# Optimization experiments

Hardware: AMD Instinct MI355X
Metric: run time of the kernel (lower is better)

Reference implementation:

```python
import jax, jax.numpy as jnp
import numpy as np
import math

B, N, D_IN, D_V, H, D_FF = 8, 2048, 256, 256, 8, 512
HD = D_V // H  # head dim = 32
EPS = 1e-5


def layernorm(x, g, b):
    mu = jnp.mean(x, axis=-1, keepdims=True)
    var = jnp.mean(jnp.square(x - mu), axis=-1, keepdims=True)
    return (x - mu) * jax.lax.rsqrt(var + EPS) * g + b


def setup_inputs() -> dict:
    key = jax.random.key(0)
    ks = jax.random.split(key, 12)
    s = 1.0 / math.sqrt(D_IN)
    return {
        "x": jax.random.normal(ks[0], (B, N, D_IN), jnp.float32),
        "y": jax.random.normal(ks[1], (B, N, D_IN), jnp.float32),
        "Wq": jax.random.normal(ks[2], (D_IN, D_V), jnp.float32) * s,
        "bq": jnp.zeros((D_V,), jnp.float32),
        "Wk": jax.random.normal(ks[3], (D_IN, D_V), jnp.float32) * s,
        "bk": jnp.zeros((D_V,), jnp.float32),
        "Wv": jax.random.normal(ks[4], (D_IN, D_V), jnp.float32) * s,
        "bv": jnp.zeros((D_V,), jnp.float32),
        "W1": jax.random.normal(ks[5], (D_V, D_FF), jnp.float32) * s,
        "b1": jnp.zeros((D_FF,), jnp.float32),
        "W2": jax.random.normal(ks[6], (D_FF, D_V), jnp.float32) * (1.0 / math.sqrt(D_FF)),
        "b2": jnp.zeros((D_V,), jnp.float32),
        "ln0_g": jnp.ones((D_IN,), jnp.float32),
        "ln0_b": jnp.zeros((D_IN,), jnp.float32),
        "ln1_g": jnp.ones((D_V,), jnp.float32),
        "ln1_b": jnp.zeros((D_V,), jnp.float32),
    }


def reference(x, y, Wq, bq, Wk, bk, Wv, bv, W1, b1, W2, b2, ln0_g, ln0_b, ln1_g, ln1_b):
    xn = layernorm(x, ln0_g, ln0_b)                      # ln0 on queries
    Q = (xn @ Wq + bq).reshape(B, N, H, HD)              # [B,Nq,H,hd]
    K = (y @ Wk + bk).reshape(B, N, H, HD)
    V = (y @ Wv + bv).reshape(B, N, H, HD)
    # NOTE: faithful scale = 1/sqrt(dim_V) (full model dim), not head dim
    S = jnp.einsum("bqhd,bkhd->bhqk", Q, K) / math.sqrt(D_V)
    A = jax.nn.softmax(S, axis=-1)
    O = Q + jnp.einsum("bhqk,bkhd->bqhd", A, V)          # per-head residual Q_ + A
    O = O.reshape(B, N, D_V)
    On = layernorm(O, ln1_g, ln1_b)
    ff = jax.nn.gelu(On @ W1 + b1, approximate=False) @ W2 + b2
    return O + ff
```

## Files before the change

kernel.cpp:

```cpp
#include <hip/hip_runtime.h>
#include <math.h>

#define RTOT 16384
#define NSEQ 2048
#define NHEAD 8
#define HDIM 32
#define QSCALE 0.09017132252479462f
#define QINV (1.0f / QSCALE)

typedef __attribute__((ext_vector_type(8))) short short8;
typedef __attribute__((ext_vector_type(4))) float f32x4;

#define GLOBAL_AS(p) ((__attribute__((address_space(1))) void*)(p))
#define LDS_AS(p) ((__attribute__((address_space(3))) void*)(p))

__device__ __forceinline__ unsigned pack_bf16(float a, float b) {
  unsigned ua = __float_as_uint(a) + 0x8000u;
  unsigned ub = __float_as_uint(b) + 0x8000u;
  return (ua >> 16) | (ub & 0xffff0000u);
}
__device__ __forceinline__ unsigned pack_bf16_perm(float a, float b) {
  return __builtin_amdgcn_perm(__float_as_uint(b), __float_as_uint(a),
                               0x07060302u);
}
__device__ __forceinline__ ushort bf16_1(float a) {
  return (ushort)((__float_as_uint(a) + 0x8000u) >> 16);
}
__device__ __forceinline__ float bf16_to_f(ushort u) {
  return __uint_as_float(((unsigned)u) << 16);
}

__global__ __launch_bounds__(256) void stage0_kernel(
    const float* __restrict__ x, const float* __restrict__ y,
    const float* __restrict__ Wq, const float* __restrict__ Wk,
    const float* __restrict__ Wv, const float* __restrict__ W1,
    const float* __restrict__ W2, const float* __restrict__ ln0g,
    const float* __restrict__ ln0b, ushort* __restrict__ Wqt,
    ushort* __restrict__ Wkt, ushort* __restrict__ Wvt,
    ushort* __restrict__ W1t, ushort* __restrict__ W2t,
    ushort* __restrict__ yh, ushort* __restrict__ xh) {
  const int bid = blockIdx.x;
  const int t = threadIdx.x;
  if (bid < 112) {
    const float* W;
    ushort* Wt;
    int K, N, tile;
    if (bid < 16) { W = Wq; Wt = Wqt; K = 256; N = 256; tile = bid; }
    else if (bid < 32) { W = Wk; Wt = Wkt; K = 256; N = 256; tile = bid - 16; }
    else if (bid < 48) { W = Wv; Wt = Wvt; K = 256; N = 256; tile = bid - 32; }
    else if (bid < 80) { W = W1; Wt = W1t; K = 256; N = 512; tile = bid - 48; }
    else { W = W2; Wt = W2t; K = 512; N = 256; tile = bid - 80; }
    const int tn = N >> 6;
    const int k0 = (tile / tn) << 6, n0 = (tile % tn) << 6;
    __shared__ float T[64][65];
#pragma unroll
    for (int i = 0; i < 16; ++i) {
      const int idx = t + i * 256;
      const int r = idx >> 6, c = idx & 63;
      T[r][c] = W[(size_t)(k0 + r) * N + n0 + c];
    }
    __syncthreads();
#pragma unroll
    for (int i = 0; i < 16; ++i) {
      const int idx = t + i * 256;
      const int r = idx >> 6, c = idx & 63;
      Wt[(size_t)(n0 + r) * K + k0 + c] = bf16_1(T[c][r]);
    }
  } else if (bid < 4208) {
    const size_t i = ((size_t)(bid - 112) * 256 + t) * 4;
    const float4 v = *(const float4*)&y[i];
    uint2 pk;
    pk.x = pack_bf16(v.x, v.y);
    pk.y = pack_bf16(v.z, v.w);
    *(uint2*)&yh[i] = pk;
  } else {
    const int lane = t & 63, wave = t >> 6;
    const size_t row = (size_t)(bid - 4208) * 4 + wave;
    const float* xr = x + row * 256;
    float4 v = *(const float4*)&xr[lane * 4];
    float s = v.x + v.y + v.z + v.w;
#pragma unroll
    for (int m = 1; m < 64; m <<= 1) s += __shfl_xor(s, m, 64);
    const float mu = s * (1.0f / 256.0f);
    const float dx = v.x - mu, dy = v.y - mu, dz = v.z - mu, dw = v.w - mu;
    float ss = dx * dx + dy * dy + dz * dz + dw * dw;
#pragma unroll
    for (int m = 1; m < 64; m <<= 1) ss += __shfl_xor(ss, m, 64);
    const float rstd = rsqrtf(ss * (1.0f / 256.0f) + 1e-5f);
    const float4 gv = *(const float4*)&ln0g[lane * 4];
    const float4 bv = *(const float4*)&ln0b[lane * 4];
    uint2 pk;
    pk.x = pack_bf16(dx * rstd * gv.x + bv.x, dy * rstd * gv.y + bv.y);
    pk.y = pack_bf16(dz * rstd * gv.z + bv.z, dw * rstd * gv.w + bv.w);
    *(uint2*)&xh[row * 256 + lane * 4] = pk;
  }
}

__global__ __launch_bounds__(256) void ln_kernel(
    const float* __restrict__ X, const float* __restrict__ g,
    const float* __restrict__ bt, ushort* __restrict__ Yh) {
  const int lane = threadIdx.x & 63;
  const int wave = threadIdx.x >> 6;
  const size_t row = (size_t)blockIdx.x * 4 + wave;
  const float* xr = X + row * 256;
  float4 v = *(const float4*)&xr[lane * 4];
  float s = v.x + v.y + v.z + v.w;
#pragma unroll
  for (int m = 1; m < 64; m <<= 1) s += __shfl_xor(s, m, 64);
  const float mu = s * (1.0f / 256.0f);
  const float dx = v.x - mu, dy = v.y - mu, dz = v.z - mu, dw = v.w - mu;
  float ss = dx * dx + dy * dy + dz * dz + dw * dw;
#pragma unroll
  for (int m = 1; m < 64; m <<= 1) ss += __shfl_xor(ss, m, 64);
  const float rstd = rsqrtf(ss * (1.0f / 256.0f) + 1e-5f);
  const float4 gv = *(const float4*)&g[lane * 4];
  const float4 bv = *(const float4*)&bt[lane * 4];
  uint2 pk;
  pk.x = pack_bf16(dx * rstd * gv.x + bv.x, dy * rstd * gv.y + bv.y);
  pk.y = pack_bf16(dz * rstd * gv.z + bv.z, dw * rstd * gv.w + bv.w);
  *(uint2*)&Yh[row * 256 + lane * 4] = pk;
}

__global__ __launch_bounds__(256) void qkv_kernel(
    const ushort* __restrict__ xh, const ushort* __restrict__ yh,
    const ushort* __restrict__ Wqt, const ushort* __restrict__ Wkt,
    const ushort* __restrict__ Wvt, const float* __restrict__ bq,
    const float* __restrict__ bk, const float* __restrict__ bv,
    ushort* __restrict__ Qh, ushort* __restrict__ Kh,
    ushort* __restrict__ VhT) {
  __shared__ union UU {
    struct { ushort As[128 * 32]; ushort Bs[64 * 32]; } s;
    ushort Ct[64 * 136];
  } u;
  const int t = threadIdx.x;
  const int lane = t & 63, wave = t >> 6;
  const int l16 = lane & 15, quad = lane >> 4;
  const int row0 = blockIdx.x * 128;
  const int ny = blockIdx.y;
  const int which = ny >> 2;
  const int n0 = (ny & 3) << 6;
  const ushort* A = (which == 2) ? xh : yh;
  const ushort* W = (which == 0) ? Wkt : (which == 1) ? Wvt : Wqt;
  const float* bs = (which == 0) ? bk : (which == 1) ? bv : bq;
  const int mrow = (wave & 1) * 64, ncol = (wave >> 1) * 32;

  const ushort* gA0 = A + (size_t)(row0 + (t >> 2)) * 256 + ((t & 3) << 3);
  const ushort* gA1 = gA0 + (size_t)64 * 256;
  const ushort* gB = W + (size_t)(n0 + (t >> 2)) * 256 + ((t & 3) << 3);
  ushort* lA0 = u.s.As + 8 * t;
  ushort* lA1 = u.s.As + 2048 + 8 * t;
  ushort* lB = u.s.Bs + 8 * t;

  f32x4 acc[4][2] = {};
  for (int kc = 0; kc < 256; kc += 32) {
    __builtin_amdgcn_global_load_lds(GLOBAL_AS(gA0 + kc), LDS_AS(lA0), 16, 0, 0);
    __builtin_amdgcn_global_load_lds(GLOBAL_AS(gA1 + kc), LDS_AS(lA1), 16, 0, 0);
    __builtin_amdgcn_global_load_lds(GLOBAL_AS(gB + kc), LDS_AS(lB), 16, 0, 0);
    __syncthreads();
    short8 af[4], bfr[2];
#pragma unroll
    for (int mi = 0; mi < 4; ++mi)
      af[mi] = *(const short8*)&u.s.As[(mrow + mi * 16 + l16) * 32 + quad * 8];
#pragma unroll
    for (int nj = 0; nj < 2; ++nj)
      bfr[nj] = *(const short8*)&u.s.Bs[(ncol + nj * 16 + l16) * 32 + quad * 8];
#pragma unroll
    for (int mi = 0; mi < 4; ++mi)
#pragma unroll
      for (int nj = 0; nj < 2; ++nj)
        acc[mi][nj] = __builtin_amdgcn_mfma_f32_16x16x32_bf16(
            af[mi], bfr[nj], acc[mi][nj], 0, 0, 0);
    __syncthreads();
  }

  if (which == 1) {
#pragma unroll
    for (int nj = 0; nj < 2; ++nj) {
      const int nloc = ncol + nj * 16 + l16;
      const float bvv = bs[n0 + nloc];
#pragma unroll
      for (int mi = 0; mi < 4; ++mi)
#pragma unroll
        for (int r = 0; r < 4; ++r)
          u.Ct[nloc * 136 + mrow + mi * 16 + quad * 4 + r] =
              bf16_1(acc[mi][nj][r] + bvv);
    }
    __syncthreads();
    const int bb = row0 >> 11, ns0 = row0 & 2047;
#pragma unroll
    for (int i = 0; i < 4; ++i) {
      const int c = t + i * 256;
      const int rr = c >> 4, c8 = (c & 15) << 3;
      *(float4*)&VhT[(size_t)(bb * 256 + n0 + rr) * 2048 + ns0 + c8] =
          *(const float4*)&u.Ct[rr * 136 + c8];
    }
  } else {
#pragma unroll
    for (int nj = 0; nj < 2; ++nj) {
      const int n = n0 + ncol + nj * 16 + l16;
      const float bvv = bs[n];
#pragma unroll
      for (int mi = 0; mi < 4; ++mi) {
#pragma unroll
        for (int r = 0; r < 4; ++r) {
          const size_t m = (size_t)row0 + mrow + mi * 16 + quad * 4 + r;
          const float v = acc[mi][nj][r] + bvv;
          if (which == 2) Qh[m * 256 + n] = bf16_1(v * QSCALE);
          else Kh[m * 256 + n] = bf16_1(v);
        }
      }
    }
  }
}

template <int MODE>
__global__ __launch_bounds__(256) void mgemm_kernel(
    const ushort* __restrict__ A, const ushort* __restrict__ Wt,
    const float* __restrict__ bias, const float* __restrict__ res,
    float* __restrict__ Cf, ushort* __restrict__ Ch, int K, int N) {
  __shared__ ushort As[128 * 32];
  __shared__ ushort Bs[64 * 32];
  const int t = threadIdx.x;
  const int lane = t & 63, wave = t >> 6;
  const int l16 = lane & 15, quad = lane >> 4;
  const int row0 = blockIdx.x * 128;
  const int n0 = blockIdx.y << 6;
  const int mrow = (wave & 1) * 64, ncol = (wave >> 1) * 32;

  const ushort* gA0 = A + (size_t)(row0 + (t >> 2)) * K + ((t & 3) << 3);
  const ushort* gA1 = gA0 + (size_t)64 * K;
  const ushort* gB = Wt + (size_t)(n0 + (t >> 2)) * K + ((t & 3) << 3);
  ushort* lA0 = As + 8 * t;
  ushort* lA1 = As + 2048 + 8 * t;
  ushort* lB = Bs + 8 * t;

  f32x4 acc[4][2] = {};
  for (int kc = 0; kc < K; kc += 32) {
    __builtin_amdgcn_global_load_lds(GLOBAL_AS(gA0 + kc), LDS_AS(lA0), 16, 0, 0);
    __builtin_amdgcn_global_load_lds(GLOBAL_AS(gA1 + kc), LDS_AS(lA1), 16, 0, 0);
    __builtin_amdgcn_global_load_lds(GLOBAL_AS(gB + kc), LDS_AS(lB), 16, 0, 0);
    __syncthreads();
    short8 af[4], bfr[2];
#pragma unroll
    for (int mi = 0; mi < 4; ++mi)
      af[mi] = *(const short8*)&As[(mrow + mi * 16 + l16) * 32 + quad * 8];
#pragma unroll
    for (int nj = 0; nj < 2; ++nj)
      bfr[nj] = *(const short8*)&Bs[(ncol + nj * 16 + l16) * 32 + quad * 8];
#pragma unroll
    for (int mi = 0; mi < 4; ++mi)
#pragma unroll
      for (int nj = 0; nj < 2; ++nj)
        acc[mi][nj] = __builtin_amdgcn_mfma_f32_16x16x32_bf16(
            af[mi], bfr[nj], acc[mi][nj], 0, 0, 0);
    __syncthreads();
  }
#pragma unroll
  for (int nj = 0; nj < 2; ++nj) {
    const int n = n0 + ncol + nj * 16 + l16;
    const float bvv = bias[n];
#pragma unroll
    for (int mi = 0; mi < 4; ++mi) {
#pragma unroll
      for (int r = 0; r < 4; ++r) {
        const size_t m = (size_t)row0 + mrow + mi * 16 + quad * 4 + r;
        float v = acc[mi][nj][r] + bvv;
        if (MODE == 2) {
          v = 0.5f * v * (1.0f + erff(v * 0.70710678118654752f));
          Ch[m * N + n] = bf16_1(v);
        }
        if (MODE == 3) Cf[m * N + n] = v + res[m * N + n];
      }
    }
  }
}

__global__ __launch_bounds__(256) void attn_kernel(
    const ushort* __restrict__ Qh, const ushort* __restrict__ Kh,
    const ushort* __restrict__ VhT, float* __restrict__ O) {
  __shared__ ushort Ks[2][64][40];
  __shared__ ushort Vt[2][32][72];
  __shared__ ushort Pl[4][2][16][72];

  const int t = threadIdx.x;
  const int lane = t & 63, wave = t >> 6;
  const int l16 = lane & 15, quad = lane >> 4;
  const int bh = blockIdx.x & 63;
  const int qt = blockIdx.x >> 6;
  const int b = bh >> 3, h = bh & 7;

  const size_t rowQ0 = (size_t)(b * NSEQ + qt * 128 + wave * 32 + l16);
  const short8 qfrag0 = *(const short8*)&Qh[rowQ0 * 256 + h * HDIM + quad * 8];
  const short8 qfrag1 =
      *(const short8*)&Qh[(rowQ0 + 16) * 256 + h * HDIM + quad * 8];
  const short8 ones = {16256, 16256, 16256, 16256,
                       16256, 16256, 16256, 16256};
  const f32x4 zf = {0.f, 0.f, 0.f, 0.f};

  f32x4 o00 = zf, o01 = zf, o10 = zf, o11 = zf;
  f32x4 s0 = zf, s1 = zf;

  const int kr = t >> 2, kc8 = (t & 3) << 3;
  const int vd = t >> 3, vc8 = (t & 7) << 3;
  const ushort* gK = Kh + ((size_t)(b * NSEQ + kr)) * 256 + h * HDIM + kc8;
  const ushort* gV = VhT + ((size_t)(bh * 32 + vd)) * 2048 + vc8;

  float4 kreg = *(const float4*)gK;
  float4 vreg = *(const float4*)gV;

  for (int kt = 0; kt < 32; ++kt) {
    const int bf = kt & 1;
    *(float4*)&Ks[bf][kr][kc8] = kreg;
    *(float4*)&Vt[bf][vd][vc8] = vreg;
    __syncthreads();
    if (kt < 31) {
      kreg = *(const float4*)(gK + (size_t)(kt + 1) * 64 * 256);
      vreg = *(const float4*)(gV + (kt + 1) * 64);
    }

    short8 kf[4];
#pragma unroll
    for (int sub = 0; sub < 4; ++sub)
      kf[sub] = *(const short8*)&Ks[bf][sub * 16 + l16][quad * 8];
    const short8 vf00 = *(const short8*)&Vt[bf][l16][quad * 8];
    const short8 vf01 = *(const short8*)&Vt[bf][l16][32 + quad * 8];
    const short8 vf10 = *(const short8*)&Vt[bf][16 + l16][quad * 8];
    const short8 vf11 = *(const short8*)&Vt[bf][16 + l16][32 + quad * 8];

    f32x4 sa0[4], sa1[4];
#pragma unroll
    for (int sub = 0; sub < 4; ++sub)
      sa0[sub] =
          __builtin_amdgcn_mfma_f32_16x16x32_bf16(kf[sub], qfrag0, zf, 0, 0, 0);
#pragma unroll
    for (int sub = 0; sub < 4; ++sub)
      sa1[sub] =
          __builtin_amdgcn_mfma_f32_16x16x32_bf16(kf[sub], qfrag1, zf, 0, 0, 0);

#pragma unroll
    for (int sub = 0; sub < 4; ++sub) {
      uint2 pk;
      pk.x = pack_bf16_perm(__builtin_amdgcn_exp2f(sa0[sub][0]),
                            __builtin_amdgcn_exp2f(sa0[sub][1]));
      pk.y = pack_bf16_perm(__builtin_amdgcn_exp2f(sa0[sub][2]),
                            __builtin_amdgcn_exp2f(sa0[sub][3]));
      *(uint2*)&Pl[wave][0][l16][sub * 16 + quad * 4] = pk;
    }
#pragma unroll
    for (int sub = 0; sub < 4; ++sub) {
      uint2 pk;
      pk.x = pack_bf16_perm(__builtin_amdgcn_exp2f(sa1[sub][0]),
                            __builtin_amdgcn_exp2f(sa1[sub][1]));
      pk.y = pack_bf16_perm(__builtin_amdgcn_exp2f(sa1[sub][2]),
                            __builtin_amdgcn_exp2f(sa1[sub][3]));
      *(uint2*)&Pl[wave][1][l16][sub * 16 + quad * 4] = pk;
    }
    __threadfence_block();

    const short8 pf00 = *(const short8*)&Pl[wave][0][l16][quad * 8];
    const short8 pf01 = *(const short8*)&Pl[wave][0][l16][32 + quad * 8];
    const short8 pf10 = *(const short8*)&Pl[wave][1][l16][quad * 8];
    const short8 pf11 = *(const short8*)&Pl[wave][1][l16][32 + quad * 8];
    o00 = __builtin_amdgcn_mfma_f32_16x16x32_bf16(pf00, vf00, o00, 0, 0, 0);
    o00 = __builtin_amdgcn_mfma_f32_16x16x32_bf16(pf01, vf01, o00, 0, 0, 0);
    o01 = __builtin_amdgcn_mfma_f32_16x16x32_bf16(pf00, vf10, o01, 0, 0, 0);
    o01 = __builtin_amdgcn_mfma_f32_16x16x32_bf16(pf01, vf11, o01, 0, 0, 0);
    o10 = __builtin_amdgcn_mfma_f32_16x16x32_bf16(pf10, vf00, o10, 0, 0, 0);
    o10 = __builtin_amdgcn_mfma_f32_16x16x32_bf16(pf11, vf01, o10, 0, 0, 0);
    o11 = __builtin_amdgcn_mfma_f32_16x16x32_bf16(pf10, vf10, o11, 0, 0, 0);
    o11 = __builtin_amdgcn_mfma_f32_16x16x32_bf16(pf11, vf11, o11, 0, 0, 0);
    s0 = __builtin_amdgcn_mfma_f32_16x16x32_bf16(pf00, ones, s0, 0, 0, 0);
    s0 = __builtin_amdgcn_mfma_f32_16x16x32_bf16(pf01, ones, s0, 0, 0, 0);
    s1 = __builtin_amdgcn_mfma_f32_16x16x32_bf16(pf10, ones, s1, 0, 0, 0);
    s1 = __builtin_amdgcn_mfma_f32_16x16x32_bf16(pf11, ones, s1, 0, 0, 0);
  }

  __threadfence_block();
  *(short8*)&Pl[wave][0][l16][quad * 8] = qfrag0;
  *(short8*)&Pl[wave][1][l16][quad * 8] = qfrag1;
  __threadfence_block();
#pragma unroll
  for (int g = 0; g < 2; ++g) {
    const f32x4 oS = g ? s1 : s0;
    const f32x4 oa = g ? o10 : o00;
    const f32x4 ob = g ? o11 : o01;
    const size_t row0 =
        (size_t)(b * NSEQ + qt * 128 + wave * 32 + g * 16 + quad * 4);
#pragma unroll
    for (int r = 0; r < 4; ++r) {
      const float q0 = bf16_to_f(Pl[wave][g][quad * 4 + r][l16]) * QINV;
      const float q1 = bf16_to_f(Pl[wave][g][quad * 4 + r][16 + l16]) * QINV;
      const float il = 1.0f / oS[r];
      const size_t ro = (row0 + r) * 256 + h * HDIM + l16;
      O[ro] = q0 + oa[r] * il;
      O[ro + 16] = q1 + ob[r] * il;
    }
  }
}

extern "C" void kernel_launch(void* const* d_in, const int* in_sizes, int n_in,
                              void* d_out, int out_size, void* d_ws, size_t ws_size,
                              hipStream_t stream) {
  const float* x = (const float*)d_in[0];
  const float* y = (const float*)d_in[1];
  const float* Wq = (const float*)d_in[2];
  const float* bq = (const float*)d_in[3];
  const float* Wk = (const float*)d_in[4];
  const float* bk = (const float*)d_in[5];
  const float* Wv = (const float*)d_in[6];
  const float* bv = (const float*)d_in[7];
  const float* W1 = (const float*)d_in[8];
  const float* b1 = (const float*)d_in[9];
  const float* W2 = (const float*)d_in[10];
  const float* b2 = (const float*)d_in[11];
  const float* ln0g = (const float*)d_in[12];
  const float* ln0b = (const float*)d_in[13];
  const float* ln1g = (const float*)d_in[14];
  const float* ln1b = (const float*)d_in[15];
  float* out = (float*)d_out;
  char* base = (char*)d_ws;

  const size_t RM = (size_t)RTOT * 256;
  ushort* yh = (ushort*)base;
  float* Ob = (float*)base;
  ushort* Qh = (ushort*)(base + 2 * RM * 4);
  ushort* Kh = (ushort*)(base + 2 * RM * 4 + RM * 2);
  ushort* VhT = (ushort*)(base + 3 * RM * 4);
  ushort* xh = (ushort*)(base + 3 * RM * 4 + RM * 2);
  ushort* Onh = xh;
  ushort* Hidh = Qh;
  char* wbase = base + 4 * RM * 4;
  ushort* Wqt = (ushort*)wbase;
  ushort* Wkt = Wqt + 65536;
  ushort* Wvt = Wkt + 65536;
  ushort* W1t = Wvt + 65536;
  ushort* W2t = W1t + 131072;

  stage0_kernel<<<8304, 256, 0, stream>>>(x, y, Wq, Wk, Wv, W1, W2, ln0g, ln0b,
                                          Wqt, Wkt, Wvt, W1t, W2t, yh, xh);
  qkv_kernel<<<dim3(128, 12), 256, 0, stream>>>(xh, yh, Wqt, Wkt, Wvt, bq, bk,
                                                bv, Qh, Kh, VhT);
  attn_kernel<<<1024, 256, 0, stream>>>(Qh, Kh, VhT, Ob);
  ln_kernel<<<RTOT / 4, 256, 0, stream>>>(Ob, ln1g, ln1b, Onh);
  mgemm_kernel<2><<<dim3(128, 8), 256, 0, stream>>>(Onh, W1t, b1, nullptr,
                                                    nullptr, Hidh, 256, 512);
  mgemm_kernel<3><<<dim3(128, 4), 256, 0, stream>>>(Hidh, W2t, b2, Ob, out,
                                                    nullptr, 512, 256);
}
```

Baseline: 224.6 us.

## Pass softmax probabilities between MFMAs via permlane32 swap instead of LDS

The attention kernel no longer writes the exponentiated scores to a per-wave LDS buffer and reads them back as MFMA A-operands. Instead it permutes the K rows loaded into shared memory so that the S-accumulator layout, after v_permlane32_swap, lines up directly with the PV MFMA operand layout. This removes one LDS store/load round trip and a fence per key tile, and frees the Pl shared buffer. The epilogue now reuses the Ks buffer for the Q residual, which needs a __syncthreads. The whole scheme depends on the row-permutation bookkeeping being exactly right.

```diff
diff --git a/kernel.cpp b/kernel.cpp
--- a/kernel.cpp
+++ b/kernel.cpp
@@ -10,6 +10,7 @@
 
 typedef __attribute__((ext_vector_type(8))) short short8;
 typedef __attribute__((ext_vector_type(4))) float f32x4;
+typedef __attribute__((ext_vector_type(4))) unsigned uint4v;
 
 #define GLOBAL_AS(p) ((__attribute__((address_space(1))) void*)(p))
 #define LDS_AS(p) ((__attribute__((address_space(3))) void*)(p))
@@ -28,6 +29,11 @@
 }
 __device__ __forceinline__ float bf16_to_f(ushort u) {
   return __uint_as_float(((unsigned)u) << 16);
+}
+__device__ __forceinline__ short8 frag4(unsigned a0, unsigned a1, unsigned a2,
+                                        unsigned a3) {
+  uint4v t = {a0, a1, a2, a3};
+  return __builtin_bit_cast(short8, t);
 }
 
 __global__ __launch_bounds__(256) void stage0_kernel(
@@ -280,7 +286,6 @@
     const ushort* __restrict__ VhT, float* __restrict__ O) {
   __shared__ ushort Ks[2][64][40];
   __shared__ ushort Vt[2][32][72];
-  __shared__ ushort Pl[4][2][16][72];
 
   const int t = threadIdx.x;
   const int lane = t & 63, wave = t >> 6;
@@ -301,8 +306,9 @@
   f32x4 s0 = zf, s1 = zf;
 
   const int kr = t >> 2, kc8 = (t & 3) << 3;
+  const int krL = (kr & ~12) | ((kr & 4) << 1) | ((kr & 8) >> 1);
   const int vd = t >> 3, vc8 = (t & 7) << 3;
-  const ushort* gK = Kh + ((size_t)(b * NSEQ + kr)) * 256 + h * HDIM + kc8;
+  const ushort* gK = Kh + ((size_t)(b * NSEQ + krL)) * 256 + h * HDIM + kc8;
   const ushort* gV = VhT + ((size_t)(bh * 32 + vd)) * 2048 + vc8;
 
   float4 kreg = *(const float4*)gK;
@@ -337,30 +343,43 @@
       sa1[sub] =
           __builtin_amdgcn_mfma_f32_16x16x32_bf16(kf[sub], qfrag1, zf, 0, 0, 0);
 
+    unsigned p0[4][2], p1[4][2];
 #pragma unroll
     for (int sub = 0; sub < 4; ++sub) {
-      uint2 pk;
-      pk.x = pack_bf16_perm(__builtin_amdgcn_exp2f(sa0[sub][0]),
-                            __builtin_amdgcn_exp2f(sa0[sub][1]));
-      pk.y = pack_bf16_perm(__builtin_amdgcn_exp2f(sa0[sub][2]),
-                            __builtin_amdgcn_exp2f(sa0[sub][3]));
-      *(uint2*)&Pl[wave][0][l16][sub * 16 + quad * 4] = pk;
+      p0[sub][0] = pack_bf16_perm(__builtin_amdgcn_exp2f(sa0[sub][0]),
+                                  __builtin_amdgcn_exp2f(sa0[sub][1]));
+      p0[sub][1] = pack_bf16_perm(__builtin_amdgcn_exp2f(sa0[sub][2]),
+                                  __builtin_amdgcn_exp2f(sa0[sub][3]));
     }
 #pragma unroll
     for (int sub = 0; sub < 4; ++sub) {
-      uint2 pk;
-      pk.x = pack_bf16_perm(__builtin_amdgcn_exp2f(sa1[sub][0]),
-                            __builtin_amdgcn_exp2f(sa1[sub][1]));
-      pk.y = pack_bf16_perm(__builtin_amdgcn_exp2f(sa1[sub][2]),
-                            __builtin_amdgcn_exp2f(sa1[sub][3]));
-      *(uint2*)&Pl[wave][1][l16][sub * 16 + quad * 4] = pk;
-    }
-    __threadfence_block();
-
-    const short8 pf00 = *(const short8*)&Pl[wave][0][l16][quad * 8];
-    const short8 pf01 = *(const short8*)&Pl[wave][0][l16][32 + quad * 8];
-    const short8 pf10 = *(const short8*)&Pl[wave][1][l16][quad * 8];
-    const short8 pf11 = *(const short8*)&Pl[wave][1][l16][32 + quad * 8];
+      p1[sub][0] = pack_bf16_perm(__builtin_amdgcn_exp2f(sa1[sub][0]),
+                                  __builtin_amdgcn_exp2f(sa1[sub][1]));
+      p1[sub][1] = pack_bf16_perm(__builtin_amdgcn_exp2f(sa1[sub][2]),
+                                  __builtin_amdgcn_exp2f(sa1[sub][3]));
+    }
+    unsigned u00 = p0[0][0], w00 = p0[1][0];
+    asm("v_permlane32_swap_b32 %0, %1" : "+v"(u00), "+v"(w00));
+    unsigned u01 = p0[0][1], w01 = p0[1][1];
+    asm("v_permlane32_swap_b32 %0, %1" : "+v"(u01), "+v"(w01));
+    unsigned u02 = p0[2][0], w02 = p0[3][0];
+    asm("v_permlane32_swap_b32 %0, %1" : "+v"(u02), "+v"(w02));
+    unsigned u03 = p0[2][1], w03 = p0[3][1];
+    asm("v_permlane32_swap_b32 %0, %1" : "+v"(u03), "+v"(w03));
+    const short8 pf00 = frag4(u00, u01, w00, w01);
+    const short8 pf01 = frag4(u02, u03, w02, w03);
+
+    unsigned u10 = p1[0][0], w10 = p1[1][0];
+    asm("v_permlane32_swap_b32 %0, %1" : "+v"(u10), "+v"(w10));
+    unsigned u11 = p1[0][1], w11 = p1[1][1];
+    asm("v_permlane32_swap_b32 %0, %1" : "+v"(u11), "+v"(w11));
+    unsigned u12 = p1[2][0], w12 = p1[3][0];
+    asm("v_permlane32_swap_b32 %0, %1" : "+v"(u12), "+v"(w12));
+    unsigned u13 = p1[2][1], w13 = p1[3][1];
+    asm("v_permlane32_swap_b32 %0, %1" : "+v"(u13), "+v"(w13));
+    const short8 pf10 = frag4(u10, u11, w10, w11);
+    const short8 pf11 = frag4(u12, u13, w12, w13);
+
     o00 = __builtin_amdgcn_mfma_f32_16x16x32_bf16(pf00, vf00, o00, 0, 0, 0);
     o00 = __builtin_amdgcn_mfma_f32_16x16x32_bf16(pf01, vf01, o00, 0, 0, 0);
     o01 = __builtin_amdgcn_mfma_f32_16x16x32_bf16(pf00, vf10, o01, 0, 0, 0);
@@ -375,21 +394,23 @@
     s1 = __builtin_amdgcn_mfma_f32_16x16x32_bf16(pf11, ones, s1, 0, 0, 0);
   }
 
-  __threadfence_block();
-  *(short8*)&Pl[wave][0][l16][quad * 8] = qfrag0;
-  *(short8*)&Pl[wave][1][l16][quad * 8] = qfrag1;
+  __syncthreads();
+  ushort* sc = (ushort*)Ks + wave * 1280;
+  *(short8*)&sc[l16 * 40 + quad * 8] = qfrag0;
+  *(short8*)&sc[640 + l16 * 40 + quad * 8] = qfrag1;
   __threadfence_block();
 #pragma unroll
   for (int g = 0; g < 2; ++g) {
     const f32x4 oS = g ? s1 : s0;
     const f32x4 oa = g ? o10 : o00;
     const f32x4 ob = g ? o11 : o01;
+    const ushort* scg = sc + g * 640;
     const size_t row0 =
         (size_t)(b * NSEQ + qt * 128 + wave * 32 + g * 16 + quad * 4);
 #pragma unroll
     for (int r = 0; r < 4; ++r) {
-      const float q0 = bf16_to_f(Pl[wave][g][quad * 4 + r][l16]) * QINV;
-      const float q1 = bf16_to_f(Pl[wave][g][quad * 4 + r][16 + l16]) * QINV;
+      const float q0 = bf16_to_f(scg[(quad * 4 + r) * 40 + l16]) * QINV;
+      const float q1 = bf16_to_f(scg[(quad * 4 + r) * 40 + 16 + l16]) * QINV;
       const float il = 1.0f / oS[r];
       const size_t ro = (row0 + r) * 256 + h * HDIM + l16;
       O[ro] = q0 + oa[r] * il;
```

Result: faster. 218.8 us (-2.6%).

## Keep attention probabilities in registers via permlane swap, halve query tile per wave

Applied to the files above, without the earlier changes.

The attention kernel no longer round-trips softmax probabilities through LDS. K rows are loaded in a permuted order so the score MFMA output, after v_permlane32_swap, lines up directly as the A operand of the PV MFMA. Each wave now handles 16 query rows instead of 32, the grid doubles to 2048 blocks, launch bounds request 8 blocks per CU, and s_setprio is raised around the PV MFMAs. The Q residual is read back from global memory in the epilogue. This removes LDS traffic and fences per tile, but halves K/V reuse per block and doubles the global K/V loads.

```diff
diff --git a/kernel.cpp b/kernel.cpp
--- a/kernel.cpp
+++ b/kernel.cpp
@@ -10,6 +10,7 @@
 
 typedef __attribute__((ext_vector_type(8))) short short8;
 typedef __attribute__((ext_vector_type(4))) float f32x4;
+typedef __attribute__((ext_vector_type(4))) unsigned uint4v;
 
 #define GLOBAL_AS(p) ((__attribute__((address_space(1))) void*)(p))
 #define LDS_AS(p) ((__attribute__((address_space(3))) void*)(p))
@@ -28,6 +29,11 @@
 }
 __device__ __forceinline__ float bf16_to_f(ushort u) {
   return __uint_as_float(((unsigned)u) << 16);
+}
+__device__ __forceinline__ short8 frag4(unsigned a0, unsigned a1, unsigned a2,
+                                        unsigned a3) {
+  uint4v t = {a0, a1, a2, a3};
+  return __builtin_bit_cast(short8, t);
 }
 
 __global__ __launch_bounds__(256) void stage0_kernel(
@@ -275,12 +281,11 @@
   }
 }
 
-__global__ __launch_bounds__(256) void attn_kernel(
+__global__ __launch_bounds__(256, 8) void attn_kernel(
     const ushort* __restrict__ Qh, const ushort* __restrict__ Kh,
     const ushort* __restrict__ VhT, float* __restrict__ O) {
   __shared__ ushort Ks[2][64][40];
   __shared__ ushort Vt[2][32][72];
-  __shared__ ushort Pl[4][2][16][72];
 
   const int t = threadIdx.x;
   const int lane = t & 63, wave = t >> 6;
@@ -289,20 +294,18 @@
   const int qt = blockIdx.x >> 6;
   const int b = bh >> 3, h = bh & 7;
 
-  const size_t rowQ0 = (size_t)(b * NSEQ + qt * 128 + wave * 32 + l16);
-  const short8 qfrag0 = *(const short8*)&Qh[rowQ0 * 256 + h * HDIM + quad * 8];
-  const short8 qfrag1 =
-      *(const short8*)&Qh[(rowQ0 + 16) * 256 + h * HDIM + quad * 8];
+  const size_t rowQ = (size_t)(b * NSEQ + qt * 64 + wave * 16 + l16);
+  const short8 qfrag = *(const short8*)&Qh[rowQ * 256 + h * HDIM + quad * 8];
   const short8 ones = {16256, 16256, 16256, 16256,
                        16256, 16256, 16256, 16256};
   const f32x4 zf = {0.f, 0.f, 0.f, 0.f};
 
-  f32x4 o00 = zf, o01 = zf, o10 = zf, o11 = zf;
-  f32x4 s0 = zf, s1 = zf;
+  f32x4 oa = zf, ob = zf, sl = zf;
 
   const int kr = t >> 2, kc8 = (t & 3) << 3;
+  const int krL = (kr & ~12) | ((kr & 4) << 1) | ((kr & 8) >> 1);
   const int vd = t >> 3, vc8 = (t & 7) << 3;
-  const ushort* gK = Kh + ((size_t)(b * NSEQ + kr)) * 256 + h * HDIM + kc8;
+  const ushort* gK = Kh + ((size_t)(b * NSEQ + krL)) * 256 + h * HDIM + kc8;
   const ushort* gV = VhT + ((size_t)(bh * 32 + vd)) * 2048 + vc8;
 
   float4 kreg = *(const float4*)gK;
@@ -327,74 +330,48 @@
     const short8 vf10 = *(const short8*)&Vt[bf][16 + l16][quad * 8];
     const short8 vf11 = *(const short8*)&Vt[bf][16 + l16][32 + quad * 8];
 
-    f32x4 sa0[4], sa1[4];
+    f32x4 sa[4];
 #pragma unroll
     for (int sub = 0; sub < 4; ++sub)
-      sa0[sub] =
-          __builtin_amdgcn_mfma_f32_16x16x32_bf16(kf[sub], qfrag0, zf, 0, 0, 0);
-#pragma unroll
-    for (int sub = 0; sub < 4; ++sub)
-      sa1[sub] =
-          __builtin_amdgcn_mfma_f32_16x16x32_bf16(kf[sub], qfrag1, zf, 0, 0, 0);
-
+      sa[sub] =
+          __builtin_amdgcn_mfma_f32_16x16x32_bf16(kf[sub], qfrag, zf, 0, 0, 0);
+
+    unsigned p[4][2];
 #pragma unroll
     for (int sub = 0; sub < 4; ++sub) {
-      uint2 pk;
-      pk.x = pack_bf16_perm(__builtin_amdgcn_exp2f(sa0[sub][0]),
-                            __builtin_amdgcn_exp2f(sa0[sub][1]));
-      pk.y = pack_bf16_perm(__builtin_amdgcn_exp2f(sa0[sub][2]),
-                            __builtin_amdgcn_exp2f(sa0[sub][3]));
-      *(uint2*)&Pl[wave][0][l16][sub * 16 + quad * 4] = pk;
-    }
-#pragma unroll
-    for (int sub = 0; sub < 4; ++sub) {
-      uint2 pk;
-      pk.x = pack_bf16_perm(__builtin_amdgcn_exp2f(sa1[sub][0]),
-                            __builtin_amdgcn_exp2f(sa1[sub][1]));
-      pk.y = pack_bf16_perm(__builtin_amdgcn_exp2f(sa1[sub][2]),
-                            __builtin_amdgcn_exp2f(sa1[sub][3]));
-      *(uint2*)&Pl[wave][1][l16][sub * 16 + quad * 4] = pk;
-    }
-    __threadfence_block();
-
-    const short8 pf00 = *(const short8*)&Pl[wave][0][l16][quad * 8];
-    const short8 pf01 = *(const short8*)&Pl[wave][0][l16][32 + quad * 8];
-    const short8 pf10 = *(const short8*)&Pl[wave][1][l16][quad * 8];
-    const short8 pf11 = *(const short8*)&Pl[wave][1][l16][32 + quad * 8];
-    o00 = __builtin_amdgcn_mfma_f32_16x16x32_bf16(pf00, vf00, o00, 0, 0, 0);
-    o00 = __builtin_amdgcn_mfma_f32_16x16x32_bf16(pf01, vf01, o00, 0, 0, 0);
-    o01 = __builtin_amdgcn_mfma_f32_16x16x32_bf16(pf00, vf10, o01, 0, 0, 0);
-    o01 = __builtin_amdgcn_mfma_f32_16x16x32_bf16(pf01, vf11, o01, 0, 0, 0);
-    o10 = __builtin_amdgcn_mfma_f32_16x16x32_bf16(pf10, vf00, o10, 0, 0, 0);
-    o10 = __builtin_amdgcn_mfma_f32_16x16x32_bf16(pf11, vf01, o10, 0, 0, 0);
-    o11 = __builtin_amdgcn_mfma_f32_16x16x32_bf16(pf10, vf10, o11, 0, 0, 0);
-    o11 = __builtin_amdgcn_mfma_f32_16x16x32_bf16(pf11, vf11, o11, 0, 0, 0);
-    s0 = __builtin_amdgcn_mfma_f32_16x16x32_bf16(pf00, ones, s0, 0, 0, 0);
-    s0 = __builtin_amdgcn_mfma_f32_16x16x32_bf16(pf01, ones, s0, 0, 0, 0);
-    s1 = __builtin_amdgcn_mfma_f32_16x16x32_bf16(pf10, ones, s1, 0, 0, 0);
-    s1 = __builtin_amdgcn_mfma_f32_16x16x32_bf16(pf11, ones, s1, 0, 0, 0);
-  }
-
-  __threadfence_block();
-  *(short8*)&Pl[wave][0][l16][quad * 8] = qfrag0;
-  *(short8*)&Pl[wave][1][l16][quad * 8] = qfrag1;
-  __threadfence_block();
-#pragma unroll
-  for (int g = 0; g < 2; ++g) {
-    const f32x4 oS = g ? s1 : s0;
-    const f32x4 oa = g ? o10 : o00;
-    const f32x4 ob = g ? o11 : o01;
-    const size_t row0 =
-        (size_t)(b * NSEQ + qt * 128 + wave * 32 + g * 16 + quad * 4);
-#pragma unroll
-    for (int r = 0; r < 4; ++r) {
-      const float q0 = bf16_to_f(Pl[wave][g][quad * 4 + r][l16]) * QINV;
-      const float q1 = bf16_to_f(Pl[wave][g][quad * 4 + r][16 + l16]) * QINV;
-      const float il = 1.0f / oS[r];
-      const size_t ro = (row0 + r) * 256 + h * HDIM + l16;
-      O[ro] = q0 + oa[r] * il;
-      O[ro + 16] = q1 + ob[r] * il;
-    }
+      p[sub][0] = pack_bf16_perm(__builtin_amdgcn_exp2f(sa[sub][0]),
+                                 __builtin_amdgcn_exp2f(sa[sub][1]));
+      p[sub][1] = pack_bf16_perm(__builtin_amdgcn_exp2f(sa[sub][2]),
+                                 __builtin_amdgcn_exp2f(sa[sub][3]));
+    }
+    unsigned u0 = p[0][0], w0 = p[1][0];
+    asm("v_permlane32_swap_b32 %0, %1" : "+v"(u0), "+v"(w0));
+    unsigned u1 = p[0][1], w1 = p[1][1];
+    asm("v_permlane32_swap_b32 %0, %1" : "+v"(u1), "+v"(w1));
+    unsigned u2 = p[2][0], w2 = p[3][0];
+    asm("v_permlane32_swap_b32 %0, %1" : "+v"(u2), "+v"(w2));
+    unsigned u3 = p[2][1], w3 = p[3][1];
+    asm("v_permlane32_swap_b32 %0, %1" : "+v"(u3), "+v"(w3));
+    const short8 pf0 = frag4(u0, u1, w0, w1);
+    const short8 pf1 = frag4(u2, u3, w2, w3);
+
+    __builtin_amdgcn_s_setprio(1);
+    oa = __builtin_amdgcn_mfma_f32_16x16x32_bf16(pf0, vf00, oa, 0, 0, 0);
+    oa = __builtin_amdgcn_mfma_f32_16x16x32_bf16(pf1, vf01, oa, 0, 0, 0);
+    ob = __builtin_amdgcn_mfma_f32_16x16x32_bf16(pf0, vf10, ob, 0, 0, 0);
+    ob = __builtin_amdgcn_mfma_f32_16x16x32_bf16(pf1, vf11, ob, 0, 0, 0);
+    sl = __builtin_amdgcn_mfma_f32_16x16x32_bf16(pf0, ones, sl, 0, 0, 0);
+    sl = __builtin_amdgcn_mfma_f32_16x16x32_bf16(pf1, ones, sl, 0, 0, 0);
+    __builtin_amdgcn_s_setprio(0);
+  }
+
+  const size_t row0 = (size_t)(b * NSEQ + qt * 64 + wave * 16 + quad * 4);
+#pragma unroll
+  for (int r = 0; r < 4; ++r) {
+    const float il = 1.0f / sl[r];
+    const size_t ro = (row0 + r) * 256 + h * HDIM + l16;
+    O[ro] = bf16_to_f(Qh[ro]) * QINV + oa[r] * il;
+    O[ro + 16] = bf16_to_f(Qh[ro + 16]) * QINV + ob[r] * il;
   }
 }
 
@@ -440,7 +417,7 @@
                                           Wqt, Wkt, Wvt, W1t, W2t, yh, xh);
   qkv_kernel<<<dim3(128, 12), 256, 0, stream>>>(xh, yh, Wqt, Wkt, Wvt, bq, bk,
                                                 bv, Qh, Kh, VhT);
-  attn_kernel<<<1024, 256, 0, stream>>>(Qh, Kh, VhT, Ob);
+  attn_kernel<<<2048, 256, 0, stream>>>(Qh, Kh, VhT, Ob);
   ln_kernel<<<RTOT / 4, 256, 0, stream>>>(Ob, ln1g, ln1b, Onh);
   mgemm_kernel<2><<<dim3(128, 8), 256, 0, stream>>>(Onh, W1t, b1, nullptr,
                                                     nullptr, Hidh, 256, 512);
```

Result: slower. 249.3 us (+11.0%).
